# Kernel optimization log

Hardware: AMD Instinct MI355X
Metric: run time of the kernel (lower is better)

The kernel has to match this reference:

```python
import jax, jax.numpy as jnp
import numpy as np

N_NODES = 50000
N_EDGES = 800000
QRY = 128
KEY = 128
VAL = 128
HEADS = 8
HEAD_FEATS = VAL // HEADS
BN_EPS = 1e-5


def setup_inputs() -> dict:
    key = jax.random.key(0)
    ks = jax.random.split(key, 12)
    inp = {
        "ft_q": jax.random.normal(ks[0], (N_NODES, QRY), dtype=jnp.float32),
        "ft_k": jax.random.normal(ks[1], (N_NODES, KEY), dtype=jnp.float32),
        "src": jax.random.randint(ks[2], (N_EDGES,), 0, N_NODES, dtype=jnp.int32),
        "dst": jax.random.randint(ks[3], (N_EDGES,), 0, N_NODES, dtype=jnp.int32),
        # learned params
        "Wq": jax.random.normal(ks[4], (VAL, QRY), dtype=jnp.float32) / np.sqrt(QRY),
        "bq": jnp.zeros((VAL,), dtype=jnp.float32),
        "Wk": jax.random.normal(ks[5], (VAL, KEY), dtype=jnp.float32) / np.sqrt(KEY),
        "Wv": jax.random.normal(ks[6], (VAL, QRY), dtype=jnp.float32) / np.sqrt(QRY),
        "attn_e": jax.random.normal(ks[7], (VAL,), dtype=jnp.float32),
        "bn_q_g": jnp.ones((QRY,), dtype=jnp.float32),
        "bn_q_b": jnp.zeros((QRY,), dtype=jnp.float32),
        "bn_k_g": jnp.ones((KEY,), dtype=jnp.float32),
        "bn_k_b": jnp.zeros((KEY,), dtype=jnp.float32),
    }
    return inp


def _batch_norm(x, gamma, beta):
    # training-mode BatchNorm1d: normalize over batch dim
    mean = jnp.mean(x, axis=0, keepdims=True)
    var = jnp.var(x, axis=0, keepdims=True)
    return (x - mean) * jax.lax.rsqrt(var + BN_EPS) * gamma + beta


def reference(ft_q, ft_k, src, dst, Wq, bq, Wk, Wv, attn_e,
              bn_q_g, bn_q_b, bn_k_g, bn_k_b):
    ft_q = _batch_norm(ft_q, bn_q_g, bn_q_b)
    ft_k = _batch_norm(ft_k, bn_k_g, bn_k_b)

    q = ft_q @ Wq.T + bq                      # [N, VAL]
    k = ft_k @ Wk.T                           # [N, VAL]
    v = (ft_q @ Wv.T).reshape(-1, HEADS, HEAD_FEATS)  # [N, H, D]

    # u_add_v: per-edge e = q[src] + k[dst]
    e = q[src] + k[dst]                       # [E, VAL]
    e = (attn_e * jax.nn.sigmoid(e)).reshape(-1, HEADS, HEAD_FEATS).sum(-1)  # [E, H]

    # edge_softmax grouped by destination node
    m = jax.ops.segment_max(e, dst, num_segments=N_NODES)   # [N, H]
    ex = jnp.exp(e - m[dst])                                # [E, H]
    s = jax.ops.segment_sum(ex, dst, num_segments=N_NODES)  # [N, H]
    a = ex / s[dst]                                         # [E, H]

    # u_mul_e_sum: scatter-sum of v[src] * a over destination
    msg = v[src] * a[:, :, None]                            # [E, H, D]
    rst = jax.ops.segment_sum(msg, dst, num_segments=N_NODES)  # [N, H, D]
    return rst.reshape(-1, VAL)
```

## Files before the change

### kernel.cpp

```cpp
#include <hip/hip_runtime.h>

#define N_NODES 50000
#define N_EDGES 800000
#define FEATS 128
#define NCHUNK 196
#define CPAD 50176
#define GEMM_BX 196
#define GEMM_BLOCKS 392
#define SCAT_BLOCKS 3125
#define NTILE 782
#define NF_WAVES 8192
#define STAT_BLOCKS 256
#define HSEG 128
#define ESEG 6250
#define HHALF 25088

typedef __attribute__((ext_vector_type(8))) short bf16x8;
typedef __attribute__((ext_vector_type(4))) float f32x4;
typedef union { uint4 u; bf16x8 v; } pack8;

__device__ __forceinline__ unsigned short f2bf(float f){
  unsigned u = __float_as_uint(f);
  u += 0x7FFF + ((u >> 16) & 1);
  return (unsigned short)(u >> 16);
}
__device__ __forceinline__ unsigned cvtpk(float lo, float hi){
  unsigned r;
  asm("v_cvt_pk_bf16_f32 %0, %1, %2" : "=v"(r) : "v"(lo), "v"(hi));
  return r;
}
__device__ __forceinline__ void unpack8(uint4 p, float* f){
  f[0]=__uint_as_float(p.x << 16); f[1]=__uint_as_float(p.x & 0xffff0000u);
  f[2]=__uint_as_float(p.y << 16); f[3]=__uint_as_float(p.y & 0xffff0000u);
  f[4]=__uint_as_float(p.z << 16); f[5]=__uint_as_float(p.z & 0xffff0000u);
  f[6]=__uint_as_float(p.w << 16); f[7]=__uint_as_float(p.w & 0xffff0000u);
}

__global__ __launch_bounds__(256) void stats_kernel(
    const float* __restrict__ ftq, const float* __restrict__ ftk,
    float* __restrict__ sums, unsigned short* __restrict__ xqb){
  __shared__ float red[4*FEATS];
  int tid = threadIdx.x, bid = blockIdx.x;
  for (int i = tid; i < 4*FEATS; i += 256) red[i] = 0.f;
  __syncthreads();
  int sub = tid >> 5, c4 = tid & 31;
  const float* Xs = (sub < 4) ? ftq : ftk;
  int so = (sub < 4) ? 0 : 2*FEATS;
  bool isq = (sub < 4);
  float a0=0,a1=0,a2=0,a3=0,b0=0,b1=0,b2=0,b3=0;
  #pragma unroll 4
  for (int r = bid*4 + (sub&3); r < N_NODES; r += STAT_BLOCKS*4){
    float4 x = *(const float4*)(Xs + (size_t)r*FEATS + c4*4);
    if (isq)
      *(uint2*)&xqb[(size_t)r*FEATS + c4*4] = make_uint2(cvtpk(x.x,x.y), cvtpk(x.z,x.w));
    a0+=x.x; b0+=x.x*x.x; a1+=x.y; b1+=x.y*x.y;
    a2+=x.z; b2+=x.z*x.z; a3+=x.w; b3+=x.w*x.w;
  }
  a0 += __shfl_xor(a0,32); a1 += __shfl_xor(a1,32);
  a2 += __shfl_xor(a2,32); a3 += __shfl_xor(a3,32);
  b0 += __shfl_xor(b0,32); b1 += __shfl_xor(b1,32);
  b2 += __shfl_xor(b2,32); b3 += __shfl_xor(b3,32);
  if ((tid & 63) < 32){
    int c0 = c4*4;
    atomicAdd(&red[so + c0+0], a0); atomicAdd(&red[so + c0+1], a1);
    atomicAdd(&red[so + c0+2], a2); atomicAdd(&red[so + c0+3], a3);
    atomicAdd(&red[so + FEATS + c0+0], b0); atomicAdd(&red[so + FEATS + c0+1], b1);
    atomicAdd(&red[so + FEATS + c0+2], b2); atomicAdd(&red[so + FEATS + c0+3], b3);
  }
  __syncthreads();
  for (int i = tid; i < 4*FEATS; i += 256) atomicAdd(&sums[i], red[i]);
}

__global__ __launch_bounds__(256) void hist_kernel(
    const int* __restrict__ dstE, unsigned short* __restrict__ rankE,
    unsigned short* __restrict__ hmat){
  __shared__ unsigned lh[HHALF/2];
  int tid = threadIdx.x, bid = blockIdx.x;
  int seg = bid >> 1, hi = bid & 1;
  int dlo = hi * HHALF;
  for (int i = tid; i < HHALF/2; i += 256) lh[i] = 0;
  __syncthreads();
  int e0 = seg * ESEG;
  for (int t = e0 + tid; t < e0 + ESEG; t += 256){
    int d = dstE[t] - dlo;
    if ((unsigned)d < (unsigned)HHALF){
      unsigned sh = (d & 1) * 16;
      unsigned old = atomicAdd(&lh[d >> 1], 1u << sh);
      rankE[t] = (unsigned short)((old >> sh) & 0xffffu);
    }
  }
  __syncthreads();
  unsigned* row = (unsigned*)(hmat + (size_t)bid * HHALF);
  for (int i = tid; i < HHALF/2; i += 256) row[i] = lh[i];
}

__global__ __launch_bounds__(256) void colscan_kernel(
    unsigned short* __restrict__ hmat, int* __restrict__ counts){
  int d = blockIdx.x*256 + threadIdx.x;
  int hi = (d >= HHALF) ? 1 : 0;
  int col = d - hi*HHALF;
  int run = 0;
  for (int s = 0; s < HSEG; s++){
    size_t idx = (size_t)(s*2 + hi)*HHALF + col;
    int v = hmat[idx];
    hmat[idx] = (unsigned short)run;
    run += v;
  }
  counts[d] = run;
}

__global__ __launch_bounds__(256) void scan_fold_kernel(
    const int* __restrict__ counts, int* __restrict__ loc, int* __restrict__ bscan,
    const float* __restrict__ Wq, const float* __restrict__ bq,
    const float* __restrict__ Wk, const float* __restrict__ Wv,
    const float* __restrict__ gq, const float* __restrict__ bqn,
    const float* __restrict__ gk, const float* __restrict__ bkn,
    const float* __restrict__ sums,
    unsigned short* __restrict__ Wb, float* __restrict__ bias){
  __shared__ int s[256];
  int tid = threadIdx.x, bid = blockIdx.x;
  if (bid < NCHUNK){
    int i = bid*256 + tid;
    int v = counts[i];
    s[tid] = v; __syncthreads();
    for (int d = 1; d < 256; d <<= 1){
      int tv = (tid >= d) ? s[tid-d] : 0; __syncthreads();
      s[tid] += tv; __syncthreads();
    }
    loc[i] = s[tid] - v;
  } else if (bid == NCHUNK){
    int total = 0;
    if (tid < NCHUNK){
      const int* cp = counts + tid*256;
      #pragma unroll 8
      for (int i = 0; i < 256; i++) total += cp[i];
    }
    s[tid] = total; __syncthreads();
    for (int d = 1; d < 256; d <<= 1){
      int tv = (tid >= d) ? s[tid-d] : 0; __syncthreads();
      s[tid] += tv; __syncthreads();
    }
    if (tid < NCHUNK) bscan[tid] = s[tid] - total;
  } else {
    int wv = (bid - NCHUNK - 1)*4 + (tid >> 6);
    int lane = tid & 63;
    int m = wv >> 7;
    int o = wv & 127;
    const float* Wsrc = (m==0) ? Wq : (m==1) ? Wv : Wk;
    const float* g   = (m==2) ? gk : gq;
    const float* bb  = (m==2) ? bkn : bqn;
    const float* s0  = (m==2) ? (sums + 2*FEATS) : sums;
    const float invN = 1.0f / (float)N_NODES;
    float acc = 0.f;
    unsigned short w2[2];
    int i0 = lane*2;
    #pragma unroll
    for (int t = 0; t < 2; t++){
      int i = i0 + t;
      float mean = s0[i]*invN;
      float var  = s0[FEATS+i]*invN - mean*mean;
      float rstd = rsqrtf(var + 1e-5f);
      float scale = g[i]*rstd;
      float shift = bb[i] - mean*scale;
      float w = Wsrc[o*FEATS + i];
      w2[t] = f2bf(w*scale);
      acc += shift*w;
    }
    ((unsigned*)Wb)[(m*FEATS*FEATS + o*FEATS + i0) >> 1] =
        (unsigned)w2[0] | ((unsigned)w2[1] << 16);
    #pragma unroll
    for (int off = 1; off < 64; off <<= 1) acc += __shfl_xor(acc, off);
    if (lane == 0) bias[m*FEATS + o] = acc + ((m==0) ? bq[o] : 0.f);
  }
}

__global__ __launch_bounds__(256) void gemm_scatter_kernel(
    const unsigned short* __restrict__ xqb, const float* __restrict__ ftk,
    const unsigned short* __restrict__ Wball, const float* __restrict__ biasall,
    unsigned short* __restrict__ qv, unsigned short* __restrict__ kb,
    const int* __restrict__ dstE, const int* __restrict__ srcE,
    const int* __restrict__ loc, const int* __restrict__ bscan,
    const unsigned short* __restrict__ rankE, const unsigned short* __restrict__ hmat,
    int* __restrict__ src_csr){
  __shared__ unsigned short Bs[2][FEATS][FEATS];
  int tid = threadIdx.x, bid = blockIdx.x;
  if (bid >= GEMM_BLOCKS){
    int t = (bid - GEMM_BLOCKS)*256 + tid;
    int d = dstE[t];
    int seg = t / ESEG;
    int hi = (d >= HHALF) ? 1 : 0;
    int base = (int)hmat[(size_t)(seg*2 + hi)*HHALF + (d - hi*HHALF)];
    src_csr[loc[d] + bscan[d >> 8] + base + (int)rankE[t]] = srcE[t];
    return;
  }
  int isk = (bid >= GEMM_BX);
  int bx = isk ? bid - GEMM_BX : bid;
  int nplanes = isk ? 1 : 2;
  {
    for (int p = 0; p < nplanes; p++){
      int m = isk ? 2 : p;
      const uint4* srcp = (const uint4*)(Wball + m*FEATS*FEATS);
      for (int idx = tid; idx < FEATS*FEATS/8; idx += 256){
        int n = idx >> 4, ck = idx & 15;
        *(uint4*)&Bs[p][n][(ck ^ (n & 15))*8] = srcp[idx];
      }
    }
  }
  __syncthreads();
  int wave = tid >> 6, lane = tid & 63;
  int mrow = lane & 15, quad = lane >> 4;
  float bv[2][8];
  #pragma unroll
  for (int p = 0; p < 2; p++)
    #pragma unroll
    for (int ct = 0; ct < 8; ct++)
      bv[p][ct] = biasall[(isk ? 2 : p)*FEATS + ct*16 + mrow];
  uint4 cur[4], nxt[4];
  auto loadA = [&](uint4* buf, int t){
    int arow = t*64 + wave*16 + mrow;
    if (!isk){
      const unsigned short* xp = xqb + (size_t)arow*FEATS + quad*8;
      buf[0] = *(const uint4*)xp;
      buf[1] = *(const uint4*)(xp + 32);
      buf[2] = *(const uint4*)(xp + 64);
      buf[3] = *(const uint4*)(xp + 96);
    } else {
      bool rok = arow < N_NODES;
      const float* xp = ftk + (size_t)(rok ? arow : 0)*FEATS + quad*8;
      #pragma unroll
      for (int kt = 0; kt < 4; kt++){
        float4 x0 = *(const float4*)(xp + kt*32);
        float4 x1 = *(const float4*)(xp + kt*32 + 4);
        if (!rok){ x0 = make_float4(0.f,0.f,0.f,0.f); x1 = x0; }
        buf[kt].x = cvtpk(x0.x, x0.y); buf[kt].y = cvtpk(x0.z, x0.w);
        buf[kt].z = cvtpk(x1.x, x1.y); buf[kt].w = cvtpk(x1.z, x1.w);
      }
    }
  };
  loadA(cur, bx);
  for (int t = bx; t < NTILE; t += GEMM_BX){
    int tn = t + GEMM_BX;
    if (tn < NTILE) loadA(nxt, tn);
    f32x4 acc[2][8];
    #pragma unroll
    for (int p = 0; p < 2; p++)
      #pragma unroll
      for (int i = 0; i < 8; i++) acc[p][i] = (f32x4){0.f,0.f,0.f,0.f};
    #pragma unroll
    for (int kt = 0; kt < 4; kt++){
      pack8 a; a.u = cur[kt];
      #pragma unroll
      for (int ct = 0; ct < 8; ct++){
        bf16x8 b0 = *(bf16x8*)&Bs[0][ct*16 + mrow][((kt*4 + quad) ^ mrow)*8];
        acc[0][ct] = __builtin_amdgcn_mfma_f32_16x16x32_bf16(a.v, b0, acc[0][ct], 0, 0, 0);
      }
      if (!isk){
        #pragma unroll
        for (int ct = 0; ct < 8; ct++){
          bf16x8 b1 = *(bf16x8*)&Bs[1][ct*16 + mrow][((kt*4 + quad) ^ mrow)*8];
          acc[1][ct] = __builtin_amdgcn_mfma_f32_16x16x32_bf16(a.v, b1, acc[1][ct], 0, 0, 0);
        }
      }
    }
    int row0 = t*64;
    #pragma unroll
    for (int p = 0; p < 2; p++){
      if (isk && p) break;
      unsigned short* Out = isk ? kb : (qv + p*128);
      const int ostride = isk ? FEATS : 256;
      #pragma unroll
      for (int ct = 0; ct < 8; ct++){
        int col = ct*16 + mrow;
        #pragma unroll
        for (int v = 0; v < 4; v++){
          int orow = row0 + wave*16 + quad*4 + v;
          float s = acc[p][ct][v] + bv[p][ct];
          float pf = __shfl_xor(s, 1);
          if (!(mrow & 1) && orow < N_NODES)
            *(unsigned*)&Out[(size_t)orow*ostride + col] = cvtpk(s, pf);
        }
      }
    }
    #pragma unroll
    for (int i = 0; i < 4; i++) cur[i] = nxt[i];
  }
}

__global__ __launch_bounds__(256) void node_fused_kernel(
    const unsigned short* __restrict__ qv, const unsigned short* __restrict__ kb,
    const float* __restrict__ attn, const int* __restrict__ src_csr,
    const int* __restrict__ loc, const int* __restrict__ bscan,
    float* __restrict__ out){
  int tid = threadIdx.x;
  int lane = tid & 63;
  int h = lane & 7, g = lane >> 3;
  int w = blockIdx.x*4 + (tid >> 6);
  const float L2E = 1.44269504f;
  float ar[16];
  {
    const uint4* ap = (const uint4*)(attn + h*16);
    uint4 a0 = ap[0], a1 = ap[1], a2 = ap[2], a3 = ap[3];
    ar[0]=__uint_as_float(a0.x); ar[1]=__uint_as_float(a0.y); ar[2]=__uint_as_float(a0.z); ar[3]=__uint_as_float(a0.w);
    ar[4]=__uint_as_float(a1.x); ar[5]=__uint_as_float(a1.y); ar[6]=__uint_as_float(a1.z); ar[7]=__uint_as_float(a1.w);
    ar[8]=__uint_as_float(a2.x); ar[9]=__uint_as_float(a2.y); ar[10]=__uint_as_float(a2.z); ar[11]=__uint_as_float(a2.w);
    ar[12]=__uint_as_float(a3.x); ar[13]=__uint_as_float(a3.y); ar[14]=__uint_as_float(a3.z); ar[15]=__uint_as_float(a3.w);
  }
  for (int n = w; n < N_NODES; n += NF_WAVES){
    int off0 = loc[n]   + bscan[n>>8];
    int off1 = loc[n+1] + bscan[(n+1)>>8];
    int deg = off1 - off0;
    if (deg == 0){
      ((float2*)(out + (size_t)n*FEATS))[lane] = make_float2(0.f, 0.f);
      continue;
    }
    float kf2[16];
    {
      const unsigned short* kr = kb + (size_t)n*FEATS + h*16;
      uint4 k0 = *(const uint4*)kr;
      uint4 k1 = *(const uint4*)(kr + 8);
      float kf[16]; unpack8(k0, kf); unpack8(k1, kf+8);
      #pragma unroll
      for (int i = 0; i < 16; i++) kf2[i] = -L2E * kf[i];
    }
    float ssum = 0.f;
    float acc[16];
    #pragma unroll
    for (int i = 0; i < 16; i++) acc[i] = 0.f;
    if (g < deg){
      int sA = src_csr[off0 + g];
      int jB = g + 8;
      int sB = (jB < deg) ? src_csr[off0 + jB] : sA;
      const unsigned short* pA = qv + (size_t)sA*256 + h*16;
      uint4 qa0 = *(const uint4*)pA;
      uint4 qa1 = *(const uint4*)(pA + 8);
      while (true){
        uint4 va0 = *(const uint4*)(pA + 128);
        uint4 va1 = *(const uint4*)(pA + 136);
        const unsigned short* pB = qv + (size_t)sB*256 + h*16;
        uint4 qb0 = *(const uint4*)pB;
        uint4 qb1 = *(const uint4*)(pB + 8);
        int jC = jB + 8;
        int sC = (jC < deg) ? src_csr[off0 + jC] : sB;
        float qf[16]; unpack8(qa0, qf); unpack8(qa1, qf+8);
        float ta = 0.f, tb = 0.f, tc = 0.f, td = 0.f;
        #pragma unroll
        for (int i = 0; i < 16; i += 4){
          float x0 = fmaf(qf[i+0], -L2E, kf2[i+0]);
          float x1 = fmaf(qf[i+1], -L2E, kf2[i+1]);
          float x2 = fmaf(qf[i+2], -L2E, kf2[i+2]);
          float x3 = fmaf(qf[i+3], -L2E, kf2[i+3]);
          ta = fmaf(ar[i+0], __builtin_amdgcn_rcpf(1.f + __builtin_amdgcn_exp2f(x0)), ta);
          tb = fmaf(ar[i+1], __builtin_amdgcn_rcpf(1.f + __builtin_amdgcn_exp2f(x1)), tb);
          tc = fmaf(ar[i+2], __builtin_amdgcn_rcpf(1.f + __builtin_amdgcn_exp2f(x2)), tc);
          td = fmaf(ar[i+3], __builtin_amdgcn_rcpf(1.f + __builtin_amdgcn_exp2f(x3)), td);
        }
        float t = (ta + tb) + (tc + td);
        float ex = __builtin_amdgcn_exp2f(t * L2E);
        ssum += ex;
        float vf[16]; unpack8(va0, vf); unpack8(va1, vf+8);
        #pragma unroll
        for (int i = 0; i < 16; i++) acc[i] = fmaf(ex, vf[i], acc[i]);
        if (jB >= deg) break;
        qa0 = qb0; qa1 = qb1; pA = pB;
        jB = jC; sB = sC;
      }
    }
    ssum += __shfl_xor(ssum, 8); ssum += __shfl_xor(ssum, 16); ssum += __shfl_xor(ssum, 32);
    #pragma unroll
    for (int i = 0; i < 16; i++){
      acc[i] += __shfl_xor(acc[i], 8);
      acc[i] += __shfl_xor(acc[i], 16);
      acc[i] += __shfl_xor(acc[i], 32);
    }
    if (g == 0){
      float inv_s = 1.f / ssum;
      float4* op = (float4*)(out + (size_t)n*FEATS + h*16);
      op[0] = make_float4(acc[0]*inv_s, acc[1]*inv_s, acc[2]*inv_s, acc[3]*inv_s);
      op[1] = make_float4(acc[4]*inv_s, acc[5]*inv_s, acc[6]*inv_s, acc[7]*inv_s);
      op[2] = make_float4(acc[8]*inv_s, acc[9]*inv_s, acc[10]*inv_s, acc[11]*inv_s);
      op[3] = make_float4(acc[12]*inv_s, acc[13]*inv_s, acc[14]*inv_s, acc[15]*inv_s);
    }
  }
}

extern "C" void kernel_launch(void* const* d_in, const int* in_sizes, int n_in,
                              void* d_out, int out_size, void* d_ws, size_t ws_size,
                              hipStream_t stream){
  (void)in_sizes; (void)n_in; (void)out_size; (void)ws_size;
  const float* ftq  = (const float*)d_in[0];
  const float* ftk  = (const float*)d_in[1];
  const int*   srcE = (const int*)d_in[2];
  const int*   dstE = (const int*)d_in[3];
  const float* Wq   = (const float*)d_in[4];
  const float* bq   = (const float*)d_in[5];
  const float* Wk   = (const float*)d_in[6];
  const float* Wv   = (const float*)d_in[7];
  const float* attn = (const float*)d_in[8];
  const float* gq   = (const float*)d_in[9];
  const float* bqn  = (const float*)d_in[10];
  const float* gk   = (const float*)d_in[11];
  const float* bkn  = (const float*)d_in[12];

  char* ws = (char*)d_ws;
  float* sums    = (float*)(ws + 0);
  int*   counts  = (int*)(ws + 2048);
  int*   loc     = (int*)(ws + 202752);
  int*   bscan   = (int*)(ws + 403456);
  int*   src_csr = (int*)(ws + 404240);
  unsigned short* rankE = (unsigned short*)(ws + 3604240);
  unsigned short* hmat  = (unsigned short*)(ws + 5204240);
  unsigned short* Wb    = (unsigned short*)(ws + 18049296);
  float* biasf   = (float*)(ws + 18147600);
  unsigned short* xqb = (unsigned short*)(ws + 18149152);
  unsigned short* qv  = (unsigned short*)(ws + 30994208);
  unsigned short* kb  = (unsigned short*)(ws + 56594208);
  float* out = (float*)d_out;

  hipMemsetAsync(ws, 0, 2048, stream);

  hipLaunchKernelGGL(stats_kernel, dim3(STAT_BLOCKS), dim3(256), 0, stream,
                     ftq, ftk, sums, xqb);
  hipLaunchKernelGGL(hist_kernel, dim3(2*HSEG), dim3(256), 0, stream,
                     dstE, rankE, hmat);
  hipLaunchKernelGGL(colscan_kernel, dim3(NCHUNK), dim3(256), 0, stream,
                     hmat, counts);
  hipLaunchKernelGGL(scan_fold_kernel, dim3(293), dim3(256), 0, stream,
                     counts, loc, bscan,
                     Wq, bq, Wk, Wv, gq, bqn, gk, bkn, sums, Wb, biasf);
  hipLaunchKernelGGL(gemm_scatter_kernel, dim3(GEMM_BLOCKS + SCAT_BLOCKS), dim3(256), 0, stream,
                     xqb, ftk, Wb, biasf, qv, kb, dstE, srcE, loc, bscan, rankE, hmat, src_csr);
  hipLaunchKernelGGL(node_fused_kernel, dim3(NF_WAVES/4), dim3(256), 0, stream,
                     qv, kb, attn, src_csr, loc, bscan, out);
}
```

Before: 281.5 us.

## Merge stats with histogram, fuse column scan into fold, split scatter from GEMM

Runs the BN statistics and destination histogram as one launch, with disjoint block ranges doing each job. The per-column prefix over segments is folded into the local-scan kernel, which writes bases to a separate buffer and emits per-chunk sums. A tiny single-block kernel then scans those sums. The edge scatter and the GEMM go back to being separate launches. The aim is to cut the serialized launch chain and the extra passes over counts, at the cost of one more small launch and a larger workspace.

Measured after the change: 267.1 us. 5.1% less time.

```diff
diff --git a/kernel.cpp b/kernel.cpp
--- a/kernel.cpp
+++ b/kernel.cpp
@@ -36,81 +36,67 @@
   f[6]=__uint_as_float(p.w << 16); f[7]=__uint_as_float(p.w & 0xffff0000u);
 }
 
-__global__ __launch_bounds__(256) void stats_kernel(
+__global__ __launch_bounds__(256) void stats_hist_kernel(
     const float* __restrict__ ftq, const float* __restrict__ ftk,
-    float* __restrict__ sums, unsigned short* __restrict__ xqb){
-  __shared__ float red[4*FEATS];
-  int tid = threadIdx.x, bid = blockIdx.x;
-  for (int i = tid; i < 4*FEATS; i += 256) red[i] = 0.f;
-  __syncthreads();
-  int sub = tid >> 5, c4 = tid & 31;
-  const float* Xs = (sub < 4) ? ftq : ftk;
-  int so = (sub < 4) ? 0 : 2*FEATS;
-  bool isq = (sub < 4);
-  float a0=0,a1=0,a2=0,a3=0,b0=0,b1=0,b2=0,b3=0;
-  #pragma unroll 4
-  for (int r = bid*4 + (sub&3); r < N_NODES; r += STAT_BLOCKS*4){
-    float4 x = *(const float4*)(Xs + (size_t)r*FEATS + c4*4);
-    if (isq)
-      *(uint2*)&xqb[(size_t)r*FEATS + c4*4] = make_uint2(cvtpk(x.x,x.y), cvtpk(x.z,x.w));
-    a0+=x.x; b0+=x.x*x.x; a1+=x.y; b1+=x.y*x.y;
-    a2+=x.z; b2+=x.z*x.z; a3+=x.w; b3+=x.w*x.w;
-  }
-  a0 += __shfl_xor(a0,32); a1 += __shfl_xor(a1,32);
-  a2 += __shfl_xor(a2,32); a3 += __shfl_xor(a3,32);
-  b0 += __shfl_xor(b0,32); b1 += __shfl_xor(b1,32);
-  b2 += __shfl_xor(b2,32); b3 += __shfl_xor(b3,32);
-  if ((tid & 63) < 32){
-    int c0 = c4*4;
-    atomicAdd(&red[so + c0+0], a0); atomicAdd(&red[so + c0+1], a1);
-    atomicAdd(&red[so + c0+2], a2); atomicAdd(&red[so + c0+3], a3);
-    atomicAdd(&red[so + FEATS + c0+0], b0); atomicAdd(&red[so + FEATS + c0+1], b1);
-    atomicAdd(&red[so + FEATS + c0+2], b2); atomicAdd(&red[so + FEATS + c0+3], b3);
-  }
-  __syncthreads();
-  for (int i = tid; i < 4*FEATS; i += 256) atomicAdd(&sums[i], red[i]);
-}
-
-__global__ __launch_bounds__(256) void hist_kernel(
+    float* __restrict__ sums, unsigned short* __restrict__ xqb,
     const int* __restrict__ dstE, unsigned short* __restrict__ rankE,
     unsigned short* __restrict__ hmat){
+  __shared__ float red[4*FEATS];
   __shared__ unsigned lh[HHALF/2];
   int tid = threadIdx.x, bid = blockIdx.x;
-  int seg = bid >> 1, hi = bid & 1;
-  int dlo = hi * HHALF;
-  for (int i = tid; i < HHALF/2; i += 256) lh[i] = 0;
-  __syncthreads();
-  int e0 = seg * ESEG;
-  for (int t = e0 + tid; t < e0 + ESEG; t += 256){
-    int d = dstE[t] - dlo;
-    if ((unsigned)d < (unsigned)HHALF){
-      unsigned sh = (d & 1) * 16;
-      unsigned old = atomicAdd(&lh[d >> 1], 1u << sh);
-      rankE[t] = (unsigned short)((old >> sh) & 0xffffu);
-    }
-  }
-  __syncthreads();
-  unsigned* row = (unsigned*)(hmat + (size_t)bid * HHALF);
-  for (int i = tid; i < HHALF/2; i += 256) row[i] = lh[i];
-}
-
-__global__ __launch_bounds__(256) void colscan_kernel(
-    unsigned short* __restrict__ hmat, int* __restrict__ counts){
-  int d = blockIdx.x*256 + threadIdx.x;
-  int hi = (d >= HHALF) ? 1 : 0;
-  int col = d - hi*HHALF;
-  int run = 0;
-  for (int s = 0; s < HSEG; s++){
-    size_t idx = (size_t)(s*2 + hi)*HHALF + col;
-    int v = hmat[idx];
-    hmat[idx] = (unsigned short)run;
-    run += v;
-  }
-  counts[d] = run;
-}
-
-__global__ __launch_bounds__(256) void scan_fold_kernel(
-    const int* __restrict__ counts, int* __restrict__ loc, int* __restrict__ bscan,
+  if (bid < STAT_BLOCKS){
+    for (int i = tid; i < 4*FEATS; i += 256) red[i] = 0.f;
+    __syncthreads();
+    int sub = tid >> 5, c4 = tid & 31;
+    const float* Xs = (sub < 4) ? ftq : ftk;
+    int so = (sub < 4) ? 0 : 2*FEATS;
+    bool isq = (sub < 4);
+    float a0=0,a1=0,a2=0,a3=0,b0=0,b1=0,b2=0,b3=0;
+    #pragma unroll 4
+    for (int r = bid*4 + (sub&3); r < N_NODES; r += STAT_BLOCKS*4){
+      float4 x = *(const float4*)(Xs + (size_t)r*FEATS + c4*4);
+      if (isq)
+        *(uint2*)&xqb[(size_t)r*FEATS + c4*4] = make_uint2(cvtpk(x.x,x.y), cvtpk(x.z,x.w));
+      a0+=x.x; b0+=x.x*x.x; a1+=x.y; b1+=x.y*x.y;
+      a2+=x.z; b2+=x.z*x.z; a3+=x.w; b3+=x.w*x.w;
+    }
+    a0 += __shfl_xor(a0,32); a1 += __shfl_xor(a1,32);
+    a2 += __shfl_xor(a2,32); a3 += __shfl_xor(a3,32);
+    b0 += __shfl_xor(b0,32); b1 += __shfl_xor(b1,32);
+    b2 += __shfl_xor(b2,32); b3 += __shfl_xor(b3,32);
+    if ((tid & 63) < 32){
+      int c0 = c4*4;
+      atomicAdd(&red[so + c0+0], a0); atomicAdd(&red[so + c0+1], a1);
+      atomicAdd(&red[so + c0+2], a2); atomicAdd(&red[so + c0+3], a3);
+      atomicAdd(&red[so + FEATS + c0+0], b0); atomicAdd(&red[so + FEATS + c0+1], b1);
+      atomicAdd(&red[so + FEATS + c0+2], b2); atomicAdd(&red[so + FEATS + c0+3], b3);
+    }
+    __syncthreads();
+    for (int i = tid; i < 4*FEATS; i += 256) atomicAdd(&sums[i], red[i]);
+  } else {
+    int hb = bid - STAT_BLOCKS;
+    int seg = hb >> 1, hi = hb & 1;
+    int dlo = hi * HHALF;
+    for (int i = tid; i < HHALF/2; i += 256) lh[i] = 0;
+    __syncthreads();
+    int e0 = seg * ESEG;
+    for (int t = e0 + tid; t < e0 + ESEG; t += 256){
+      int d = dstE[t] - dlo;
+      if ((unsigned)d < (unsigned)HHALF){
+        unsigned sh = (d & 1) * 16;
+        unsigned old = atomicAdd(&lh[d >> 1], 1u << sh);
+        rankE[t] = (unsigned short)((old >> sh) & 0xffffu);
+      }
+    }
+    __syncthreads();
+    unsigned* row = (unsigned*)(hmat + (size_t)hb * HHALF);
+    for (int i = tid; i < HHALF/2; i += 256) row[i] = lh[i];
+  }
+}
+
+__global__ __launch_bounds__(256) void colscan_fold_kernel(
+    const unsigned short* __restrict__ hmat, unsigned short* __restrict__ hbase,
+    int* __restrict__ loc, int* __restrict__ csums,
     const float* __restrict__ Wq, const float* __restrict__ bq,
     const float* __restrict__ Wk, const float* __restrict__ Wv,
     const float* __restrict__ gq, const float* __restrict__ bqn,
@@ -120,29 +106,27 @@
   __shared__ int s[256];
   int tid = threadIdx.x, bid = blockIdx.x;
   if (bid < NCHUNK){
-    int i = bid*256 + tid;
-    int v = counts[i];
-    s[tid] = v; __syncthreads();
-    for (int d = 1; d < 256; d <<= 1){
-      int tv = (tid >= d) ? s[tid-d] : 0; __syncthreads();
+    int d = bid*256 + tid;
+    int hi = (d >= HHALF) ? 1 : 0;
+    int col = d - hi*HHALF;
+    const unsigned short* hp = hmat + (size_t)hi*HHALF + col;
+    unsigned short* bp = hbase + (size_t)hi*HHALF + col;
+    int run = 0;
+    #pragma unroll 8
+    for (int sg = 0; sg < HSEG; sg++){
+      int v = hp[(size_t)sg*2*HHALF];
+      bp[(size_t)sg*2*HHALF] = (unsigned short)run;
+      run += v;
+    }
+    s[tid] = run; __syncthreads();
+    for (int dd = 1; dd < 256; dd <<= 1){
+      int tv = (tid >= dd) ? s[tid-dd] : 0; __syncthreads();
       s[tid] += tv; __syncthreads();
     }
-    loc[i] = s[tid] - v;
-  } else if (bid == NCHUNK){
-    int total = 0;
-    if (tid < NCHUNK){
-      const int* cp = counts + tid*256;
-      #pragma unroll 8
-      for (int i = 0; i < 256; i++) total += cp[i];
-    }
-    s[tid] = total; __syncthreads();
-    for (int d = 1; d < 256; d <<= 1){
-      int tv = (tid >= d) ? s[tid-d] : 0; __syncthreads();
-      s[tid] += tv; __syncthreads();
-    }
-    if (tid < NCHUNK) bscan[tid] = s[tid] - total;
+    loc[d] = s[tid] - run;
+    if (tid == 255) csums[bid] = s[255];
   } else {
-    int wv = (bid - NCHUNK - 1)*4 + (tid >> 6);
+    int wv = (bid - NCHUNK)*4 + (tid >> 6);
     int lane = tid & 63;
     int m = wv >> 7;
     int o = wv & 127;
@@ -174,25 +158,38 @@
   }
 }
 
-__global__ __launch_bounds__(256) void gemm_scatter_kernel(
+__global__ __launch_bounds__(256) void bscan_kernel(
+    const int* __restrict__ csums, int* __restrict__ bscan){
+  __shared__ int s[256];
+  int tid = threadIdx.x;
+  int v = (tid < NCHUNK) ? csums[tid] : 0;
+  s[tid] = v; __syncthreads();
+  for (int d = 1; d < 256; d <<= 1){
+    int tv = (tid >= d) ? s[tid-d] : 0; __syncthreads();
+    s[tid] += tv; __syncthreads();
+  }
+  if (tid < NCHUNK) bscan[tid] = s[tid] - v;
+}
+
+__global__ __launch_bounds__(256) void scatter_kernel(
+    const int* __restrict__ dstE, const int* __restrict__ srcE,
+    const int* __restrict__ loc, const int* __restrict__ bscan,
+    const unsigned short* __restrict__ rankE, const unsigned short* __restrict__ hbase,
+    int* __restrict__ src_csr){
+  int t = blockIdx.x*256 + threadIdx.x;
+  int d = dstE[t];
+  int seg = t / ESEG;
+  int hi = (d >= HHALF) ? 1 : 0;
+  int base = (int)hbase[(size_t)(seg*2 + hi)*HHALF + (d - hi*HHALF)];
+  src_csr[loc[d] + bscan[d >> 8] + base + (int)rankE[t]] = srcE[t];
+}
+
+__global__ __launch_bounds__(256) void gemm_kernel(
     const unsigned short* __restrict__ xqb, const float* __restrict__ ftk,
     const unsigned short* __restrict__ Wball, const float* __restrict__ biasall,
-    unsigned short* __restrict__ qv, unsigned short* __restrict__ kb,
-    const int* __restrict__ dstE, const int* __restrict__ srcE,
-    const int* __restrict__ loc, const int* __restrict__ bscan,
-    const unsigned short* __restrict__ rankE, const unsigned short* __restrict__ hmat,
-    int* __restrict__ src_csr){
+    unsigned short* __restrict__ qv, unsigned short* __restrict__ kb){
   __shared__ unsigned short Bs[2][FEATS][FEATS];
   int tid = threadIdx.x, bid = blockIdx.x;
-  if (bid >= GEMM_BLOCKS){
-    int t = (bid - GEMM_BLOCKS)*256 + tid;
-    int d = dstE[t];
-    int seg = t / ESEG;
-    int hi = (d >= HHALF) ? 1 : 0;
-    int base = (int)hmat[(size_t)(seg*2 + hi)*HHALF + (d - hi*HHALF)];
-    src_csr[loc[d] + bscan[d >> 8] + base + (int)rankE[t]] = srcE[t];
-    return;
-  }
   int isk = (bid >= GEMM_BX);
   int bx = isk ? bid - GEMM_BX : bid;
   int nplanes = isk ? 1 : 2;
@@ -274,10 +271,10 @@
         #pragma unroll
         for (int v = 0; v < 4; v++){
           int orow = row0 + wave*16 + quad*4 + v;
-          float s = acc[p][ct][v] + bv[p][ct];
-          float pf = __shfl_xor(s, 1);
+          float sv = acc[p][ct][v] + bv[p][ct];
+          float pf = __shfl_xor(sv, 1);
           if (!(mrow & 1) && orow < N_NODES)
-            *(unsigned*)&Out[(size_t)orow*ostride + col] = cvtpk(s, pf);
+            *(unsigned*)&Out[(size_t)orow*ostride + col] = cvtpk(sv, pf);
         }
       }
     }
@@ -403,32 +400,32 @@
 
   char* ws = (char*)d_ws;
   float* sums    = (float*)(ws + 0);
-  int*   counts  = (int*)(ws + 2048);
-  int*   loc     = (int*)(ws + 202752);
-  int*   bscan   = (int*)(ws + 403456);
-  int*   src_csr = (int*)(ws + 404240);
-  unsigned short* rankE = (unsigned short*)(ws + 3604240);
-  unsigned short* hmat  = (unsigned short*)(ws + 5204240);
-  unsigned short* Wb    = (unsigned short*)(ws + 18049296);
-  float* biasf   = (float*)(ws + 18147600);
-  unsigned short* xqb = (unsigned short*)(ws + 18149152);
-  unsigned short* qv  = (unsigned short*)(ws + 30994208);
-  unsigned short* kb  = (unsigned short*)(ws + 56594208);
+  int*   csums   = (int*)(ws + 2048);
+  int*   bscan   = (int*)(ws + 2848);
+  int*   loc     = (int*)(ws + 4096);
+  int*   src_csr = (int*)(ws + 204800);
+  unsigned short* rankE = (unsigned short*)(ws + 3404800);
+  unsigned short* hmat  = (unsigned short*)(ws + 5004800);
+  unsigned short* hbase = (unsigned short*)(ws + 17849856);
+  unsigned short* Wb    = (unsigned short*)(ws + 30694912);
+  float* biasf   = (float*)(ws + 30793216);
+  unsigned short* xqb = (unsigned short*)(ws + 30794752);
+  unsigned short* qv  = (unsigned short*)(ws + 43639808);
+  unsigned short* kb  = (unsigned short*)(ws + 69239808);
   float* out = (float*)d_out;
 
   hipMemsetAsync(ws, 0, 2048, stream);
 
-  hipLaunchKernelGGL(stats_kernel, dim3(STAT_BLOCKS), dim3(256), 0, stream,
-                     ftq, ftk, sums, xqb);
-  hipLaunchKernelGGL(hist_kernel, dim3(2*HSEG), dim3(256), 0, stream,
-                     dstE, rankE, hmat);
-  hipLaunchKernelGGL(colscan_kernel, dim3(NCHUNK), dim3(256), 0, stream,
-                     hmat, counts);
-  hipLaunchKernelGGL(scan_fold_kernel, dim3(293), dim3(256), 0, stream,
-                     counts, loc, bscan,
+  hipLaunchKernelGGL(stats_hist_kernel, dim3(2*STAT_BLOCKS), dim3(256), 0, stream,
+                     ftq, ftk, sums, xqb, dstE, rankE, hmat);
+  hipLaunchKernelGGL(colscan_fold_kernel, dim3(NCHUNK + 96), dim3(256), 0, stream,
+                     hmat, hbase, loc, csums,
                      Wq, bq, Wk, Wv, gq, bqn, gk, bkn, sums, Wb, biasf);
-  hipLaunchKernelGGL(gemm_scatter_kernel, dim3(GEMM_BLOCKS + SCAT_BLOCKS), dim3(256), 0, stream,
-                     xqb, ftk, Wb, biasf, qv, kb, dstE, srcE, loc, bscan, rankE, hmat, src_csr);
+  hipLaunchKernelGGL(bscan_kernel, dim3(1), dim3(256), 0, stream, csums, bscan);
+  hipLaunchKernelGGL(scatter_kernel, dim3(SCAT_BLOCKS), dim3(256), 0, stream,
+                     dstE, srcE, loc, bscan, rankE, hbase, src_csr);
+  hipLaunchKernelGGL(gemm_kernel, dim3(GEMM_BLOCKS), dim3(256), 0, stream,
+                     xqb, ftk, Wb, biasf, qv, kb);
   hipLaunchKernelGGL(node_fused_kernel, dim3(NF_WAVES/4), dim3(256), 0, stream,
                      qv, kb, attn, src_csr, loc, bscan, out);
 }
```
